# Kernel optimization log

Measured on AMD Instinct MI355X. Metric: run time of the kernel, lower is better.

## Reference

```python
import jax, jax.numpy as jnp
import numpy as np

B = 16384
N_HIDDEN_TYPE = 16   # n_hidden option count (first block of output columns)
N_ACTIVE_TYPE = 8
N_OUT = N_HIDDEN_TYPE + N_ACTIVE_TYPE   # 24, also LSTM input size
H = 24                                   # LSTM hidden size (hardcoded in module)
LAYER_LIMIT = 24
STEPS = 2 * LAYER_LIMIT - 1              # 47


def setup_inputs() -> dict:
    key = jax.random.key(0)
    ks = jax.random.split(key, 7)
    s = 0.1
    return {
        "W_ih": jax.random.normal(ks[0], (4 * H, N_OUT), jnp.float32) * s,
        "W_hh": jax.random.normal(ks[1], (4 * H, H), jnp.float32) * s,
        "b_ih": jax.random.normal(ks[2], (4 * H,), jnp.float32) * s,
        "b_hh": jax.random.normal(ks[3], (4 * H,), jnp.float32) * s,
        "Wl": jax.random.normal(ks[4], (N_OUT, H), jnp.float32) * s,
        "bl": jax.random.normal(ks[5], (N_OUT,), jnp.float32) * s,
        "rand": jax.random.uniform(ks[6], (STEPS, B), jnp.float32),
    }


def reference(W_ih, W_hh, b_ih, b_hh, Wl, bl, rand):
    cols = jnp.arange(N_OUT)

    def step(carry, xs):
        h, c, a = carry
        i, r = xs  # i: step index (scalar), r: (B,) uniforms
        # PyTorch LSTMCell: gate order input, forget, cell, output
        gates = a @ W_ih.T + b_ih + h @ W_hh.T + b_hh
        ig, fg, gg, og = jnp.split(gates, 4, axis=1)
        c = jax.nn.sigmoid(fg) * c + jax.nn.sigmoid(ig) * jnp.tanh(gg)
        h = jax.nn.sigmoid(og) * jnp.tanh(c)
        logits = h @ Wl.T + bl  # (B, N_OUT)
        counter = (i + 1) // 2  # counter_nb_layers at an odd step
        mask = jnp.where(i % 2 == 1, cols < counter, cols >= N_HIDDEN_TYPE)
        p = jax.nn.softmax(jnp.where(mask, logits, -jnp.inf), axis=1)
        # stochastic sampling: first index where cumsum exceeds uniform
        act = jnp.argmax(jnp.cumsum(p, axis=1) > r[:, None], axis=1)
        pr = jnp.take_along_axis(p, act[:, None], axis=1)[:, 0]
        a_next = jax.nn.one_hot(act, N_OUT, dtype=logits.dtype)
        return (h, c, a_next), (pr, act)

    h0 = jnp.zeros((B, H), jnp.float32)
    c0 = jnp.zeros((B, H), jnp.float32)
    a0 = jnp.zeros((B, N_OUT), jnp.float32)
    _, (prob, actions) = jax.lax.scan(
        step, (h0, c0, a0), (jnp.arange(STEPS), rand))
    # stack over time -> (B, STEPS), actions as float like the numpy array
    return prob.T, actions.T.astype(jnp.float32)
```

## Files before the change

kernel.cpp:

```cpp
#include <hip/hip_runtime.h>
#include <math.h>

#define BATCH   16384
#define HD      24
#define NOUTC   24
#define NHID    16
#define NSTEPS  47
#define NG      96
#define GRP     16
#define NTG     12
#define JPW     2
#define GPW     8
#define THREADS 192

__device__ __forceinline__ float fast_sigmoid(float x) {
    float t = __expf(-x);
    return __builtin_amdgcn_rcpf(1.0f + t);
}
__device__ __forceinline__ float fast_tanh(float x) {
    float ax = fabsf(x);
    float t  = __expf(-2.0f * ax);
    float r  = (1.0f - t) * __builtin_amdgcn_rcpf(1.0f + t);
    return copysignf(r, x);
}

__global__ __launch_bounds__(THREADS) void policy_kernel(
    const float* __restrict__ W_ih, const float* __restrict__ W_hh,
    const float* __restrict__ b_ih, const float* __restrict__ b_hh,
    const float* __restrict__ Wl,   const float* __restrict__ bl,
    const float* __restrict__ rnd,  float* __restrict__ out)
{
    __shared__ float sWihB[NG][25];
    __shared__ float sBias[NG];
    __shared__ float sWhhP[HD][NTG][GPW];
    __shared__ float sWlP[HD][NTG][JPW];
    __shared__ float sBl[NOUTC];
    __shared__ float hh[HD][GRP];
    __shared__ float sLt[GRP][28];
    __shared__ float sPr[GRP][NSTEPS + 2];
    __shared__ unsigned char sAct8[GRP][NSTEPS + 2];

    const int tid = threadIdx.x;
    const int w   = tid >> 4;
    const int e   = tid & 15;
    const int b   = blockIdx.x * GRP + e;

    for (int i = tid; i < NG * HD; i += THREADS) {
        int g = i / HD, k = i % HD;
        float bs = b_ih[g] + b_hh[g];
        sWihB[g][k] = W_ih[i] + bs;
        int t = g / 24, rem = g % 24;
        sWhhP[k][rem >> 1][t * JPW + (rem & 1)] = W_hh[i];
    }
    for (int i = tid; i < NOUTC * HD; i += THREADS) {
        int n = i / HD, k = i % HD;
        sWlP[k][n >> 1][n & 1] = Wl[i];
    }
    if (tid < NG)    sBias[tid] = b_ih[tid] + b_hh[tid];
    if (tid < NOUTC) sBl[tid]   = bl[tid];
    for (int i = tid; i < HD * GRP; i += THREADS) (&hh[0][0])[i] = 0.f;
    __syncthreads();

    float cst[JPW] = {0.f, 0.f};
    float accN[GPW];
    #pragma unroll
    for (int q = 0; q < GPW; ++q) accN[q] = 0.f;
    int act = 0;

    for (int s = 0; s < NSTEPS; ++s) {
        const float r = rnd[s * BATCH + b];

        float acc[GPW];
        if (s == 0) {
            #pragma unroll
            for (int t = 0; t < 4; ++t)
                #pragma unroll
                for (int i = 0; i < JPW; ++i)
                    acc[t * JPW + i] = accN[t * JPW + i] + sBias[t * 24 + w * JPW + i];
        } else {
            #pragma unroll
            for (int t = 0; t < 4; ++t)
                #pragma unroll
                for (int i = 0; i < JPW; ++i)
                    acc[t * JPW + i] = accN[t * JPW + i] + sWihB[t * 24 + w * JPW + i][act];
        }

        #pragma unroll
        for (int i = 0; i < JPW; ++i) {
            float ig = acc[i], fg = acc[JPW + i], gg = acc[2 * JPW + i], og = acc[3 * JPW + i];
            float si = fast_sigmoid(ig);
            float sf = fast_sigmoid(fg);
            float so = fast_sigmoid(og);
            float tg = fast_tanh(gg);
            float cj = sf * cst[i] + si * tg;
            cst[i] = cj;
            hh[w * JPW + i][e] = so * fast_tanh(cj);
        }
        __syncthreads();

        float l0 = 0.f, l1 = 0.f;
        #pragma unroll
        for (int q = 0; q < GPW; ++q) accN[q] = 0.f;
        #pragma unroll 6
        for (int k = 0; k < HD; ++k) {
            float hk = hh[k][e];
            const float* wp = &sWhhP[k][w][0];
            float4 w0 = *(const float4*)&wp[0];
            float4 w1 = *(const float4*)&wp[4];
            float2 lv = *(const float2*)&sWlP[k][w][0];
            accN[0] = fmaf(hk, w0.x, accN[0]);
            accN[1] = fmaf(hk, w0.y, accN[1]);
            accN[2] = fmaf(hk, w0.z, accN[2]);
            accN[3] = fmaf(hk, w0.w, accN[3]);
            accN[4] = fmaf(hk, w1.x, accN[4]);
            accN[5] = fmaf(hk, w1.y, accN[5]);
            accN[6] = fmaf(hk, w1.z, accN[6]);
            accN[7] = fmaf(hk, w1.w, accN[7]);
            l0 = fmaf(hk, lv.x, l0);
            l1 = fmaf(hk, lv.y, l1);
        }
        sLt[e][w * JPW + 0] = l0 + sBl[w * JPW + 0];
        sLt[e][w * JPW + 1] = l1 + sBl[w * JPW + 1];
        __syncthreads();

        const int  cnt = (s + 1) >> 1;
        const bool odd = (s & 1) != 0;
        float v[NOUTC];
        #pragma unroll
        for (int n4 = 0; n4 < 6; ++n4) {
            float4 vv = *(const float4*)&sLt[e][n4 * 4];
            v[n4 * 4 + 0] = vv.x; v[n4 * 4 + 1] = vv.y;
            v[n4 * 4 + 2] = vv.z; v[n4 * 4 + 3] = vv.w;
        }
        float Z = 0.f, cum = 0.f, ea = 0.f, m = -INFINITY;
        int a = 0;
        bool found = false;
        if (odd) {
            #pragma unroll
            for (int n = 0; n < NOUTC; ++n) m = fmaxf(m, (n < cnt) ? v[n] : -INFINITY);
            #pragma unroll
            for (int n = 0; n < NOUTC; ++n) v[n] = (n < cnt) ? __expf(v[n] - m) : 0.f;
            #pragma unroll
            for (int n = 0; n < NOUTC; ++n) Z += v[n];
            const float rZ = r * Z;
            #pragma unroll
            for (int n = 0; n < NOUTC; ++n) {
                cum += v[n];
                if (!found && cum > rZ) { found = true; a = n; ea = v[n]; }
            }
            if (!found) { a = 0; ea = v[0]; }
        } else {
            #pragma unroll
            for (int n = NHID; n < NOUTC; ++n) m = fmaxf(m, v[n]);
            #pragma unroll
            for (int n = NHID; n < NOUTC; ++n) v[n] = __expf(v[n] - m);
            #pragma unroll
            for (int n = NHID; n < NOUTC; ++n) Z += v[n];
            const float rZ = r * Z;
            #pragma unroll
            for (int n = NHID; n < NOUTC; ++n) {
                cum += v[n];
                if (!found && cum > rZ) { found = true; a = n; ea = v[n]; }
            }
            if (!found) { a = 0; ea = 0.f; }
        }
        float pr = ea / Z;

        if (w == 0) { sPr[e][s] = pr; sAct8[e][s] = (unsigned char)a; }
        act = a;
    }

    __syncthreads();
    const int base = blockIdx.x * GRP * NSTEPS;
    for (int i = tid; i < GRP * NSTEPS; i += THREADS) {
        int rr = i / NSTEPS, ss = i - rr * NSTEPS;
        out[base + i]                          = sPr[rr][ss];
        out[(size_t)BATCH * NSTEPS + base + i] = (float)sAct8[rr][ss];
    }
}

extern "C" void kernel_launch(void* const* d_in, const int* in_sizes, int n_in,
                              void* d_out, int out_size, void* d_ws, size_t ws_size,
                              hipStream_t stream) {
    const float* W_ih = (const float*)d_in[0];
    const float* W_hh = (const float*)d_in[1];
    const float* b_ih = (const float*)d_in[2];
    const float* b_hh = (const float*)d_in[3];
    const float* Wl   = (const float*)d_in[4];
    const float* bl   = (const float*)d_in[5];
    const float* rnd  = (const float*)d_in[6];
    float* o = (float*)d_out;

    policy_kernel<<<BATCH / GRP, THREADS, 0, stream>>>(W_ih, W_hh, b_ih, b_hh, Wl, bl, rnd, o);
}
```

Measured before the change: 170.3 us.

## Process two batch elements per thread to reuse shared-memory weight loads

Each thread now handles two batch rows instead of one, so each block covers 32 rows and launches half as many blocks. The loaded W_hh and Wl values feed FMAs for both rows, halving weight LDS traffic per row and adding instruction-level parallelism. In exchange, register pressure and per-thread serial softmax/sampling work both double, and fewer blocks are available to fill the GPU.

```diff
diff --git a/kernel.cpp b/kernel.cpp
--- a/kernel.cpp
+++ b/kernel.cpp
@@ -7,7 +7,7 @@
 #define NHID    16
 #define NSTEPS  47
 #define NG      96
-#define GRP     16
+#define GRP     32
 #define NTG     12
 #define JPW     2
 #define GPW     8
@@ -43,7 +43,7 @@
     const int tid = threadIdx.x;
     const int w   = tid >> 4;
     const int e   = tid & 15;
-    const int b   = blockIdx.x * GRP + e;
+    const int b0  = blockIdx.x * GRP + 2 * e;
 
     for (int i = tid; i < NG * HD; i += THREADS) {
         int g = i / HD, k = i % HD;
@@ -61,113 +61,133 @@
     for (int i = tid; i < HD * GRP; i += THREADS) (&hh[0][0])[i] = 0.f;
     __syncthreads();
 
-    float cst[JPW] = {0.f, 0.f};
-    float accN[GPW];
+    float cst0[JPW] = {0.f, 0.f};
+    float cst1[JPW] = {0.f, 0.f};
+    float accN0[GPW], accN1[GPW];
     #pragma unroll
-    for (int q = 0; q < GPW; ++q) accN[q] = 0.f;
-    int act = 0;
+    for (int q = 0; q < GPW; ++q) { accN0[q] = 0.f; accN1[q] = 0.f; }
+    int act0 = 0, act1 = 0;
 
     for (int s = 0; s < NSTEPS; ++s) {
-        const float r = rnd[s * BATCH + b];
-
-        float acc[GPW];
+        const float2 r2 = *(const float2*)&rnd[s * BATCH + b0];
+
+        float a0[GPW], a1[GPW];
         if (s == 0) {
             #pragma unroll
             for (int t = 0; t < 4; ++t)
                 #pragma unroll
-                for (int i = 0; i < JPW; ++i)
-                    acc[t * JPW + i] = accN[t * JPW + i] + sBias[t * 24 + w * JPW + i];
+                for (int i = 0; i < JPW; ++i) {
+                    float bb = sBias[t * 24 + w * JPW + i];
+                    a0[t * JPW + i] = accN0[t * JPW + i] + bb;
+                    a1[t * JPW + i] = accN1[t * JPW + i] + bb;
+                }
         } else {
             #pragma unroll
             for (int t = 0; t < 4; ++t)
                 #pragma unroll
-                for (int i = 0; i < JPW; ++i)
-                    acc[t * JPW + i] = accN[t * JPW + i] + sWihB[t * 24 + w * JPW + i][act];
+                for (int i = 0; i < JPW; ++i) {
+                    int g = t * 24 + w * JPW + i;
+                    a0[t * JPW + i] = accN0[t * JPW + i] + sWihB[g][act0];
+                    a1[t * JPW + i] = accN1[t * JPW + i] + sWihB[g][act1];
+                }
         }
 
         #pragma unroll
         for (int i = 0; i < JPW; ++i) {
-            float ig = acc[i], fg = acc[JPW + i], gg = acc[2 * JPW + i], og = acc[3 * JPW + i];
-            float si = fast_sigmoid(ig);
-            float sf = fast_sigmoid(fg);
-            float so = fast_sigmoid(og);
-            float tg = fast_tanh(gg);
-            float cj = sf * cst[i] + si * tg;
-            cst[i] = cj;
-            hh[w * JPW + i][e] = so * fast_tanh(cj);
+            float si0 = fast_sigmoid(a0[i]);
+            float sf0 = fast_sigmoid(a0[JPW + i]);
+            float so0 = fast_sigmoid(a0[3 * JPW + i]);
+            float tg0 = fast_tanh(a0[2 * JPW + i]);
+            float cj0 = sf0 * cst0[i] + si0 * tg0;
+            cst0[i] = cj0;
+            float si1 = fast_sigmoid(a1[i]);
+            float sf1 = fast_sigmoid(a1[JPW + i]);
+            float so1 = fast_sigmoid(a1[3 * JPW + i]);
+            float tg1 = fast_tanh(a1[2 * JPW + i]);
+            float cj1 = sf1 * cst1[i] + si1 * tg1;
+            cst1[i] = cj1;
+            float2 hv = make_float2(so0 * fast_tanh(cj0), so1 * fast_tanh(cj1));
+            *(float2*)&hh[w * JPW + i][2 * e] = hv;
         }
         __syncthreads();
 
-        float l0 = 0.f, l1 = 0.f;
+        float l00 = 0.f, l01 = 0.f, l10 = 0.f, l11 = 0.f;
         #pragma unroll
-        for (int q = 0; q < GPW; ++q) accN[q] = 0.f;
-        #pragma unroll 6
+        for (int q = 0; q < GPW; ++q) { accN0[q] = 0.f; accN1[q] = 0.f; }
+        #pragma unroll 4
         for (int k = 0; k < HD; ++k) {
-            float hk = hh[k][e];
+            float2 hk = *(const float2*)&hh[k][2 * e];
             const float* wp = &sWhhP[k][w][0];
             float4 w0 = *(const float4*)&wp[0];
             float4 w1 = *(const float4*)&wp[4];
             float2 lv = *(const float2*)&sWlP[k][w][0];
-            accN[0] = fmaf(hk, w0.x, accN[0]);
-            accN[1] = fmaf(hk, w0.y, accN[1]);
-            accN[2] = fmaf(hk, w0.z, accN[2]);
-            accN[3] = fmaf(hk, w0.w, accN[3]);
-            accN[4] = fmaf(hk, w1.x, accN[4]);
-            accN[5] = fmaf(hk, w1.y, accN[5]);
-            accN[6] = fmaf(hk, w1.z, accN[6]);
-            accN[7] = fmaf(hk, w1.w, accN[7]);
-            l0 = fmaf(hk, lv.x, l0);
-            l1 = fmaf(hk, lv.y, l1);
-        }
-        sLt[e][w * JPW + 0] = l0 + sBl[w * JPW + 0];
-        sLt[e][w * JPW + 1] = l1 + sBl[w * JPW + 1];
+            accN0[0] = fmaf(hk.x, w0.x, accN0[0]);  accN1[0] = fmaf(hk.y, w0.x, accN1[0]);
+            accN0[1] = fmaf(hk.x, w0.y, accN0[1]);  accN1[1] = fmaf(hk.y, w0.y, accN1[1]);
+            accN0[2] = fmaf(hk.x, w0.z, accN0[2]);  accN1[2] = fmaf(hk.y, w0.z, accN1[2]);
+            accN0[3] = fmaf(hk.x, w0.w, accN0[3]);  accN1[3] = fmaf(hk.y, w0.w, accN1[3]);
+            accN0[4] = fmaf(hk.x, w1.x, accN0[4]);  accN1[4] = fmaf(hk.y, w1.x, accN1[4]);
+            accN0[5] = fmaf(hk.x, w1.y, accN0[5]);  accN1[5] = fmaf(hk.y, w1.y, accN1[5]);
+            accN0[6] = fmaf(hk.x, w1.z, accN0[6]);  accN1[6] = fmaf(hk.y, w1.z, accN1[6]);
+            accN0[7] = fmaf(hk.x, w1.w, accN0[7]);  accN1[7] = fmaf(hk.y, w1.w, accN1[7]);
+            l00 = fmaf(hk.x, lv.x, l00);            l10 = fmaf(hk.y, lv.x, l10);
+            l01 = fmaf(hk.x, lv.y, l01);            l11 = fmaf(hk.y, lv.y, l11);
+        }
+        {
+            float bl0 = sBl[w * JPW + 0], bl1 = sBl[w * JPW + 1];
+            *(float2*)&sLt[2 * e + 0][w * JPW] = make_float2(l00 + bl0, l01 + bl1);
+            *(float2*)&sLt[2 * e + 1][w * JPW] = make_float2(l10 + bl0, l11 + bl1);
+        }
         __syncthreads();
 
         const int  cnt = (s + 1) >> 1;
         const bool odd = (s & 1) != 0;
-        float v[NOUTC];
         #pragma unroll
-        for (int n4 = 0; n4 < 6; ++n4) {
-            float4 vv = *(const float4*)&sLt[e][n4 * 4];
-            v[n4 * 4 + 0] = vv.x; v[n4 * 4 + 1] = vv.y;
-            v[n4 * 4 + 2] = vv.z; v[n4 * 4 + 3] = vv.w;
-        }
-        float Z = 0.f, cum = 0.f, ea = 0.f, m = -INFINITY;
-        int a = 0;
-        bool found = false;
-        if (odd) {
+        for (int elem = 0; elem < 2; ++elem) {
+            const float r = (elem == 0) ? r2.x : r2.y;
+            const int   ee = 2 * e + elem;
+            float v[NOUTC];
             #pragma unroll
-            for (int n = 0; n < NOUTC; ++n) m = fmaxf(m, (n < cnt) ? v[n] : -INFINITY);
-            #pragma unroll
-            for (int n = 0; n < NOUTC; ++n) v[n] = (n < cnt) ? __expf(v[n] - m) : 0.f;
-            #pragma unroll
-            for (int n = 0; n < NOUTC; ++n) Z += v[n];
-            const float rZ = r * Z;
-            #pragma unroll
-            for (int n = 0; n < NOUTC; ++n) {
-                cum += v[n];
-                if (!found && cum > rZ) { found = true; a = n; ea = v[n]; }
+            for (int n4 = 0; n4 < 6; ++n4) {
+                float4 vv = *(const float4*)&sLt[ee][n4 * 4];
+                v[n4 * 4 + 0] = vv.x; v[n4 * 4 + 1] = vv.y;
+                v[n4 * 4 + 2] = vv.z; v[n4 * 4 + 3] = vv.w;
             }
-            if (!found) { a = 0; ea = v[0]; }
-        } else {
-            #pragma unroll
-            for (int n = NHID; n < NOUTC; ++n) m = fmaxf(m, v[n]);
-            #pragma unroll
-            for (int n = NHID; n < NOUTC; ++n) v[n] = __expf(v[n] - m);
-            #pragma unroll
-            for (int n = NHID; n < NOUTC; ++n) Z += v[n];
-            const float rZ = r * Z;
-            #pragma unroll
-            for (int n = NHID; n < NOUTC; ++n) {
-                cum += v[n];
-                if (!found && cum > rZ) { found = true; a = n; ea = v[n]; }
+            float Z = 0.f, cum = 0.f, ea = 0.f, m = -INFINITY;
+            int a = 0;
+            bool found = false;
+            if (odd) {
+                #pragma unroll
+                for (int n = 0; n < NOUTC; ++n) m = fmaxf(m, (n < cnt) ? v[n] : -INFINITY);
+                #pragma unroll
+                for (int n = 0; n < NOUTC; ++n) v[n] = (n < cnt) ? __expf(v[n] - m) : 0.f;
+                #pragma unroll
+                for (int n = 0; n < NOUTC; ++n) Z += v[n];
+                const float rZ = r * Z;
+                #pragma unroll
+                for (int n = 0; n < NOUTC; ++n) {
+                    cum += v[n];
+                    if (!found && cum > rZ) { found = true; a = n; ea = v[n]; }
+                }
+                if (!found) { a = 0; ea = v[0]; }
+            } else {
+                #pragma unroll
+                for (int n = NHID; n < NOUTC; ++n) m = fmaxf(m, v[n]);
+                #pragma unroll
+                for (int n = NHID; n < NOUTC; ++n) v[n] = __expf(v[n] - m);
+                #pragma unroll
+                for (int n = NHID; n < NOUTC; ++n) Z += v[n];
+                const float rZ = r * Z;
+                #pragma unroll
+                for (int n = NHID; n < NOUTC; ++n) {
+                    cum += v[n];
+                    if (!found && cum > rZ) { found = true; a = n; ea = v[n]; }
+                }
+                if (!found) { a = 0; ea = 0.f; }
             }
-            if (!found) { a = 0; ea = 0.f; }
-        }
-        float pr = ea / Z;
-
-        if (w == 0) { sPr[e][s] = pr; sAct8[e][s] = (unsigned char)a; }
-        act = a;
+            float pr = ea / Z;
+            if (w == 0) { sPr[ee][s] = pr; sAct8[ee][s] = (unsigned char)a; }
+            if (elem == 0) act0 = a; else act1 = a;
+        }
     }
 
     __syncthreads();
```

Measured after the change: 199.1 us. +16.9%, slower.
